# Kernel tuning notes

Hardware: AMD Instinct MI355X
Metric: run time of the kernel (lower is better)

## Reference

```python
import jax, jax.numpy as jnp
import numpy as np

D = 127          # feature dim d
TD = D + 1       # token_dim = d + 1 = 128
H = D            # hidden_dim defaults to d
L = 2            # num_layers
EPS = 1e-6       # block eps
LN_EPS = 1e-5    # torch LayerNorm default


def _layernorm(x, w, b):
    m = jnp.mean(x, axis=-1, keepdims=True)
    v = jnp.mean(jnp.square(x - m), axis=-1, keepdims=True)
    return (x - m) * jax.lax.rsqrt(v + LN_EPS) * w + b


def _phi(x):
    return jax.nn.elu(x) + 1.0


def _gla_block(tokens, wq, wk, wv, wg_w, wg_b, wo, l1w, l1b, l2w, l2b):
    # tokens: (B, T, TD)
    x = _layernorm(tokens, l1w, l1b)
    Q = x @ wq.T                      # (B,T,H)
    K = x @ wk.T                      # (B,T,H)
    V = x @ wv.T                      # (B,T,TD)
    G = jax.nn.sigmoid(x @ wg_w.T + wg_b)
    Vg = V * G
    Qp = _phi(Q)
    Kp = _phi(K)
    # causal linear attention via cumulative outer-product state
    kv = jnp.einsum('bth,btm->bthm', Kp, Vg)   # (B,T,H,TD)
    S_kv = jnp.cumsum(kv, axis=1)
    S_k = jnp.cumsum(Kp, axis=1)
    numerator = jnp.einsum('bth,bthm->btm', Qp, S_kv)   # (B,T,TD)
    denom = jnp.maximum(jnp.einsum('bth,bth->bt', Qp, S_k), EPS)
    attn_out = numerator / denom[..., None]
    out = tokens + (attn_out @ wo.T) * 0.1
    return _layernorm(out, l2w, l2b)


def setup_inputs() -> dict:
    key = jax.random.key(0)
    ks = jax.random.split(key, 16)
    B, N = 2, 4095
    s = 0.02  # small xavier-ish gain used by the module
    inp = {
        'xs': jax.random.normal(ks[0], (B, N, D), jnp.float32),
        'ys': jax.random.normal(ks[1], (B, N), jnp.float32),
        'query_x': jax.random.normal(ks[2], (B, 1, D), jnp.float32),
        'Wq': jax.random.normal(ks[3], (L, H, TD), jnp.float32) * s,
        'Wk': jax.random.normal(ks[4], (L, H, TD), jnp.float32) * s,
        'Wv': jax.random.normal(ks[5], (L, TD, TD), jnp.float32) * s,
        'Wg_w': jax.random.normal(ks[6], (L, TD, TD), jnp.float32) * s,
        'Wg_b': jnp.zeros((L, TD), jnp.float32),
        'Wo': jax.random.normal(ks[7], (L, TD, TD), jnp.float32) * s,
        'ln1_w': jnp.ones((L, TD), jnp.float32),
        'ln1_b': jnp.zeros((L, TD), jnp.float32),
        'ln2_w': jnp.ones((L, TD), jnp.float32),
        'ln2_b': jnp.zeros((L, TD), jnp.float32),
        'pred_w': jax.random.normal(ks[8], (1, TD), jnp.float32) * 0.1,
    }
    return inp


def reference(xs, ys, query_x, Wq, Wk, Wv, Wg_w, Wg_b, Wo,
              ln1_w, ln1_b, ln2_w, ln2_b, pred_w):
    B = xs.shape[0]
    train_tokens = jnp.concatenate([xs, ys[..., None]], axis=-1)       # (B,N,TD)
    query_token = jnp.concatenate(
        [query_x, jnp.zeros((B, 1, 1), xs.dtype)], axis=-1)            # (B,1,TD)
    tokens = jnp.concatenate([train_tokens, query_token], axis=1)      # (B,T,TD)
    for l in range(L):
        tokens = _gla_block(tokens, Wq[l], Wk[l], Wv[l], Wg_w[l], Wg_b[l],
                            Wo[l], ln1_w[l], ln1_b[l], ln2_w[l], ln2_b[l])
    y_pred = tokens[:, -1, :] @ pred_w.T   # (B,1)
    return y_pred[:, 0]
```

## Files before the change

kernel.cpp:

```cpp
#include <hip/hip_runtime.h>
#include <hip/hip_bf16.h>

#define TT 4096
#define NCH 32
#define BB 2

__device__ float g_tok[(size_t)BB*TT*128];
__device__ float g_xn [(size_t)BB*TT*128];
__device__ float g_Qp [(size_t)BB*TT*128];
__device__ float g_Kp [(size_t)BB*TT*128];
__device__ float g_Vg [(size_t)BB*TT*128];
__device__ float g_Pv [(size_t)BB*TT*128];
__device__ float g_Pg [(size_t)BB*TT*128];
__device__ float g_Ssum[(size_t)BB*NCH*16384];
__device__ float g_Spre[(size_t)BB*NCH*16384];
__device__ float g_Sk [(size_t)BB*NCH*128];
__device__ float g_Skp[(size_t)BB*NCH*128];

__device__ __forceinline__ float phi_f(float x){ return x > 0.f ? x + 1.f : __expf(x); }
__device__ __forceinline__ float sigm_f(float x){ return 1.f/(1.f+__expf(-x)); }

__global__ __launch_bounds__(256) void k0_build(const float* __restrict__ xs,
                                                const float* __restrict__ ys,
                                                const float* __restrict__ qx){
  long e = (long)blockIdx.x * 256 + threadIdx.x;
  int col = (int)(e & 127);
  long r = e >> 7;
  int t = (int)(r & (TT-1));
  int b = (int)(r >> 12);
  float v;
  if (t < TT-1) {
    v = (col < 127) ? xs[((long)b*(TT-1) + t)*127 + col] : ys[(long)b*(TT-1) + t];
  } else {
    v = (col < 127) ? qx[(long)b*127 + col] : 0.f;
  }
  g_tok[e] = v;
}

__global__ __launch_bounds__(256) void k1a_ln(const float* __restrict__ lnw,
                                              const float* __restrict__ lnb){
  int tid = threadIdx.x;
  long r0 = (long)blockIdx.x * 8;
  int row = tid >> 5;
  int col = (tid & 31) << 2;
  float4 v = *(const float4*)(g_tok + (r0 + row)*128 + col);
  float s1 = v.x+v.y+v.z+v.w;
  float s2 = v.x*v.x+v.y*v.y+v.z*v.z+v.w*v.w;
  #pragma unroll
  for (int off=1; off<32; off<<=1){ s1 += __shfl_xor(s1,off); s2 += __shfl_xor(s2,off); }
  float mean = s1*(1.f/128.f);
  float var  = s2*(1.f/128.f) - mean*mean;
  float rstd = rsqrtf(var + 1e-5f);
  float4 w4 = *(const float4*)(lnw+col);
  float4 b4 = *(const float4*)(lnb+col);
  float4 o;
  o.x = (v.x-mean)*rstd*w4.x + b4.x;
  o.y = (v.y-mean)*rstd*w4.y + b4.y;
  o.z = (v.z-mean)*rstd*w4.z + b4.z;
  o.w = (v.w-mean)*rstd*w4.w + b4.w;
  *(float4*)(g_xn + (r0 + row)*128 + col) = o;
}

__global__ __launch_bounds__(256) void k1b_gemm(
    const float* __restrict__ Wq, const float* __restrict__ Wk,
    const float* __restrict__ Wv, const float* __restrict__ Wg)
{
  __shared__ float xt[128*132];
  __shared__ float wt[128*132];
  int tid = threadIdx.x;
  int mat = blockIdx.x & 3;
  long row0 = (long)(blockIdx.x >> 2) * 128;
  const float* W = (mat==0) ? Wq : (mat==1) ? Wk : (mat==2) ? Wv : Wg;
  bool isQK = (mat < 2);
  for (int i=0;i<16;i++){
    int ts = (tid & 31) + 32*(i & 3);
    int hc = (tid >> 5) + 8*(i >> 2);
    float4 v = *(const float4*)(g_xn + (row0+ts)*128 + hc*4);
    xt[(hc*4+0)*132+ts] = v.x;
    xt[(hc*4+1)*132+ts] = v.y;
    xt[(hc*4+2)*132+ts] = v.z;
    xt[(hc*4+3)*132+ts] = v.w;
  }
  for (int i=0;i<16;i++){
    int ts = (tid & 31) + 32*(i & 3);
    int hc = (tid >> 5) + 8*(i >> 2);
    int wr = isQK ? (ts < 127 ? ts : 126) : ts;
    float4 v = *(const float4*)(W + (long)wr*128 + hc*4);
    wt[(hc*4+0)*132+ts] = v.x;
    wt[(hc*4+1)*132+ts] = v.y;
    wt[(hc*4+2)*132+ts] = v.z;
    wt[(hc*4+3)*132+ts] = v.w;
  }
  __syncthreads();
  int r0 = (tid >> 4) * 8;
  int c0 = (tid & 15) * 8;
  float acc[8][8];
  #pragma unroll
  for (int i=0;i<8;i++)
    #pragma unroll
    for (int j=0;j<8;j++) acc[i][j]=0.f;
  for (int k=0;k<128;k++){
    float4 xa = *(const float4*)&xt[k*132 + r0];
    float4 xb = *(const float4*)&xt[k*132 + r0 + 4];
    float4 wa = *(const float4*)&wt[k*132 + c0];
    float4 wb = *(const float4*)&wt[k*132 + c0 + 4];
    float xr[8] = {xa.x,xa.y,xa.z,xa.w,xb.x,xb.y,xb.z,xb.w};
    float wc[8] = {wa.x,wa.y,wa.z,wa.w,wb.x,wb.y,wb.z,wb.w};
    #pragma unroll
    for (int i=0;i<8;i++)
      #pragma unroll
      for (int j=0;j<8;j++)
        acc[i][j] += xr[i]*wc[j];
  }
  long rbase = row0 + r0;
  if (isQK){
    float* dst = (mat==0) ? g_Qp : g_Kp;
    #pragma unroll
    for (int i=0;i<8;i++){
      float v[8];
      #pragma unroll
      for (int j=0;j<8;j++) v[j] = (c0+j < 127) ? phi_f(acc[i][j]) : 0.f;
      *(float4*)(dst + (rbase+i)*128 + c0)     = make_float4(v[0],v[1],v[2],v[3]);
      *(float4*)(dst + (rbase+i)*128 + c0 + 4) = make_float4(v[4],v[5],v[6],v[7]);
    }
  } else {
    float* dst = (mat==2) ? g_Pv : g_Pg;
    #pragma unroll
    for (int i=0;i<8;i++){
      *(float4*)(dst + (rbase+i)*128 + c0)     = make_float4(acc[i][0],acc[i][1],acc[i][2],acc[i][3]);
      *(float4*)(dst + (rbase+i)*128 + c0 + 4) = make_float4(acc[i][4],acc[i][5],acc[i][6],acc[i][7]);
    }
  }
}

__global__ __launch_bounds__(256) void k1c_vg(const float* __restrict__ Wgb){
  long e = ((long)blockIdx.x*256 + threadIdx.x) * 4;
  int j = (int)(e & 127);
  float4 pv = *(const float4*)(g_Pv + e);
  float4 pg = *(const float4*)(g_Pg + e);
  float4 gb = *(const float4*)(Wgb + j);
  float4 o;
  o.x = pv.x * sigm_f(pg.x + gb.x);
  o.y = pv.y * sigm_f(pg.y + gb.y);
  o.z = pv.z * sigm_f(pg.z + gb.z);
  o.w = pv.w * sigm_f(pg.w + gb.w);
  *(float4*)(g_Vg + e) = o;
}

__global__ __launch_bounds__(256) void k2_chunksum()
{
  __shared__ float vgs[16][128];
  __shared__ float kps[16][32];
  int tid = threadIdx.x;
  int ht = blockIdx.x & 3;
  int c  = (blockIdx.x >> 2) & 31;
  int b  = blockIdx.x >> 7;
  int hl = tid >> 3, mg = tid & 7, m0 = mg << 4;
  int h  = ht*32 + hl;
  float acc[16];
  #pragma unroll
  for (int i=0;i<16;i++) acc[i]=0.f;
  float sk = 0.f;
  long base = ((long)b*TT + c*128)*128;
  for (int tb=0; tb<8; tb++){
    __syncthreads();
    { int e = tid*8; int ts = e >> 7; int cc = e & 127;
      const float* s = g_Vg + base + (long)(tb*16+ts)*128 + cc;
      *(float4*)&vgs[ts][cc]   = *(const float4*)s;
      *(float4*)&vgs[ts][cc+4] = *(const float4*)(s+4); }
    { int e = tid*2; int ts = e >> 5; int hh = e & 31;
      const float* s = g_Kp + base + (long)(tb*16+ts)*128 + ht*32 + hh;
      kps[ts][hh] = s[0]; kps[ts][hh+1] = s[1]; }
    __syncthreads();
    for (int ts=0; ts<16; ts++){
      float kp = kps[ts][hl];
      sk += kp;
      #pragma unroll
      for (int i=0;i<16;i++) acc[i] += kp * vgs[ts][m0+i];
    }
  }
  long so = (((long)b*NCH + c)*128 + h)*128 + m0;
  #pragma unroll
  for (int i=0;i<16;i+=4)
    *(float4*)(g_Ssum + so + i) = make_float4(acc[i],acc[i+1],acc[i+2],acc[i+3]);
  if (mg==0) g_Sk[((long)b*NCH + c)*128 + h] = sk;
}

__global__ __launch_bounds__(256) void k3_scan()
{
  int blk = blockIdx.x % 65;
  int b   = blockIdx.x / 65;
  if (blk < 64){
    int e = blk*256 + threadIdx.x;
    float a = 0.f;
    for (int c=0;c<NCH;c++){
      long idx = ((long)b*NCH + c)*16384 + e;
      g_Spre[idx] = a;
      a += g_Ssum[idx];
    }
  } else if (threadIdx.x < 128){
    int e = threadIdx.x;
    float a = 0.f;
    for (int c=0;c<NCH;c++){
      long idx = ((long)b*NCH + c)*128 + e;
      g_Skp[idx] = a;
      a += g_Sk[idx];
    }
  }
}

__global__ __launch_bounds__(256) void k4_fused(
    const float* __restrict__ Wo,
    const float* __restrict__ ln2w, const float* __restrict__ ln2b)
{
  __shared__ float spl[16384];
  __shared__ float ktl[128*132];
  __shared__ float bufb[32*132];
  __shared__ float skl[128];
  int tid = threadIdx.x;
  int rq = blockIdx.x & 3;
  int c  = (blockIdx.x >> 2) & 31;
  int b  = blockIdx.x >> 7;
  int r0 = rq*32;
  long cbase = ((long)b*TT + c*128)*128;
  long sbase = ((long)b*NCH + c)*16384;

  for (int i=0;i<16;i++){
    int e = i*1024 + tid*4;
    *(float4*)&spl[e] = *(const float4*)(g_Spre + sbase + e);
  }
  if (tid < 128) skl[tid] = g_Skp[((long)b*NCH + c)*128 + tid];
  for (int i=0;i<4;i++){
    int e = i*1024 + tid*4;
    int row = e >> 7, cc = e & 127;
    *(float4*)&bufb[row*132+cc] = *(const float4*)(g_Qp + cbase + (long)(r0+row)*128 + cc);
  }
  for (int i=0;i<16;i++){
    int ts = (tid & 31) + 32*(i & 3);
    int hc = (tid >> 5) + 8*(i >> 2);
    float4 v = *(const float4*)(g_Kp + cbase + (long)ts*128 + hc*4);
    ktl[(hc*4+0)*132 + ts] = v.x;
    ktl[(hc*4+1)*132 + ts] = v.y;
    ktl[(hc*4+2)*132 + ts] = v.z;
    ktl[(hc*4+3)*132 + ts] = v.w;
  }
  __syncthreads();

  int row_l = tid >> 3, cg = tid & 7;
  int tq = r0 + row_l;
  long trow = (long)b*TT + c*128 + tq;
  float acc2[16], a[16];
  #pragma unroll
  for (int i=0;i<16;i++){ acc2[i]=0.f; a[i]=0.f; }
  float den_i = 0.f;
  for (int h=0;h<128;h++){
    float qv = bufb[row_l*132 + h];
    den_i += qv * skl[h];
    #pragma unroll
    for (int j=0;j<4;j++){
      float4 s4 = *(const float4*)&spl[h*128 + cg*4 + 32*j];
      float4 k4 = *(const float4*)&ktl[h*132 + cg*4 + 32*j];
      acc2[4*j+0] += qv*s4.x; acc2[4*j+1] += qv*s4.y; acc2[4*j+2] += qv*s4.z; acc2[4*j+3] += qv*s4.w;
      a[4*j+0]    += qv*k4.x; a[4*j+1]    += qv*k4.y; a[4*j+2]    += qv*k4.z; a[4*j+3]    += qv*k4.w;
    }
  }
  float den_a = 0.f;
  #pragma unroll
  for (int j=0;j<4;j++){
    #pragma unroll
    for (int k=0;k<4;k++){
      int ts = cg*4 + 32*j + k;
      if (ts > tq) a[4*j+k] = 0.f;
      den_a += a[4*j+k];
    }
  }
  den_a += __shfl_xor(den_a, 1);
  den_a += __shfl_xor(den_a, 2);
  den_a += __shfl_xor(den_a, 4);
  float inv = 1.f / fmaxf(den_i + den_a, 1e-6f);
  __syncthreads();
  #pragma unroll
  for (int j=0;j<4;j++)
    *(float4*)&bufb[row_l*132 + cg*4 + 32*j] = make_float4(a[4*j],a[4*j+1],a[4*j+2],a[4*j+3]);
  for (int i=0;i<16;i++){
    int e = i*1024 + tid*4;
    *(float4*)&ktl[e] = *(const float4*)(g_Vg + cbase + e);
  }
  __syncthreads();
  for (int ts=0; ts<128; ts++){
    float av = bufb[row_l*132 + ts];
    #pragma unroll
    for (int j=0;j<4;j++){
      float4 v4 = *(const float4*)&ktl[ts*128 + cg*4 + 32*j];
      acc2[4*j+0]+=av*v4.x; acc2[4*j+1]+=av*v4.y; acc2[4*j+2]+=av*v4.z; acc2[4*j+3]+=av*v4.w;
    }
  }
  __syncthreads();
  #pragma unroll
  for (int j=0;j<4;j++)
    *(float4*)&bufb[row_l*132 + cg*4 + 32*j] =
      make_float4(acc2[4*j]*inv, acc2[4*j+1]*inv, acc2[4*j+2]*inv, acc2[4*j+3]*inv);
  for (int i=0;i<16;i++){
    int n  = (tid & 31) + 32*(i & 3);
    int mc = (tid >> 5) + 8*(i >> 2);
    float4 v = *(const float4*)(Wo + (long)n*128 + mc*4);
    ktl[(mc*4+0)*132 + n] = v.x;
    ktl[(mc*4+1)*132 + n] = v.y;
    ktl[(mc*4+2)*132 + n] = v.z;
    ktl[(mc*4+3)*132 + n] = v.w;
  }
  __syncthreads();
  float s[16];
  #pragma unroll
  for (int i=0;i<16;i++) s[i]=0.f;
  for (int m=0;m<128;m++){
    float av = bufb[row_l*132 + m];
    #pragma unroll
    for (int j=0;j<4;j++){
      float4 w4 = *(const float4*)&ktl[m*132 + cg*4 + 32*j];
      s[4*j+0]+=av*w4.x; s[4*j+1]+=av*w4.y; s[4*j+2]+=av*w4.z; s[4*j+3]+=av*w4.w;
    }
  }
  float outv[16];
  float s1=0.f, s2=0.f;
  #pragma unroll
  for (int j=0;j<4;j++){
    float4 t4 = *(const float4*)(g_tok + trow*128 + cg*4 + 32*j);
    outv[4*j+0] = t4.x + 0.1f*s[4*j+0];
    outv[4*j+1] = t4.y + 0.1f*s[4*j+1];
    outv[4*j+2] = t4.z + 0.1f*s[4*j+2];
    outv[4*j+3] = t4.w + 0.1f*s[4*j+3];
  }
  #pragma unroll
  for (int i=0;i<16;i++){ s1 += outv[i]; s2 += outv[i]*outv[i]; }
  s1 += __shfl_xor(s1,1); s2 += __shfl_xor(s2,1);
  s1 += __shfl_xor(s1,2); s2 += __shfl_xor(s2,2);
  s1 += __shfl_xor(s1,4); s2 += __shfl_xor(s2,4);
  float mean = s1*(1.f/128.f);
  float var  = s2*(1.f/128.f) - mean*mean;
  float rstd = rsqrtf(var + 1e-5f);
  #pragma unroll
  for (int j=0;j<4;j++){
    int n = cg*4 + 32*j;
    float4 w4 = *(const float4*)(ln2w+n);
    float4 b4 = *(const float4*)(ln2b+n);
    float4 o;
    o.x = (outv[4*j+0]-mean)*rstd*w4.x + b4.x;
    o.y = (outv[4*j+1]-mean)*rstd*w4.y + b4.y;
    o.z = (outv[4*j+2]-mean)*rstd*w4.z + b4.z;
    o.w = (outv[4*j+3]-mean)*rstd*w4.w + b4.w;
    *(float4*)(g_tok + trow*128 + n) = o;
  }
}

__global__ __launch_bounds__(128) void k5_pred(const float* __restrict__ pw,
                                               float* __restrict__ out){
  __shared__ float red[2];
  int b = blockIdx.x, tid = threadIdx.x;
  float v = g_tok[((long)b*TT + TT-1)*128 + tid] * pw[tid];
  #pragma unroll
  for (int off=1; off<64; off<<=1) v += __shfl_xor(v, off);
  if ((tid & 63) == 0) red[tid>>6] = v;
  __syncthreads();
  if (tid==0) out[b] = red[0] + red[1];
}

extern "C" void kernel_launch(void* const* d_in, const int* in_sizes, int n_in,
                              void* d_out, int out_size, void* d_ws, size_t ws_size,
                              hipStream_t stream)
{
  (void)in_sizes; (void)n_in; (void)out_size; (void)d_ws; (void)ws_size;
  const float* xs   = (const float*)d_in[0];
  const float* ys   = (const float*)d_in[1];
  const float* qx   = (const float*)d_in[2];
  const float* Wq   = (const float*)d_in[3];
  const float* Wk   = (const float*)d_in[4];
  const float* Wv   = (const float*)d_in[5];
  const float* Wgw  = (const float*)d_in[6];
  const float* Wgb  = (const float*)d_in[7];
  const float* Wo   = (const float*)d_in[8];
  const float* ln1w = (const float*)d_in[9];
  const float* ln1b = (const float*)d_in[10];
  const float* ln2w = (const float*)d_in[11];
  const float* ln2b = (const float*)d_in[12];
  const float* predw= (const float*)d_in[13];

  k0_build<<<4096, 256, 0, stream>>>(xs, ys, qx);

  for (int l=0; l<2; l++){
    const float* Wq_l  = Wq  + (size_t)l*127*128;
    const float* Wk_l  = Wk  + (size_t)l*127*128;
    const float* Wv_l  = Wv  + (size_t)l*128*128;
    const float* Wgw_l = Wgw + (size_t)l*128*128;
    const float* Wgb_l = Wgb + (size_t)l*128;
    const float* Wo_l  = Wo  + (size_t)l*128*128;
    const float* l1w = ln1w + (size_t)l*128;
    const float* l1b = ln1b + (size_t)l*128;
    const float* l2w = ln2w + (size_t)l*128;
    const float* l2b = ln2b + (size_t)l*128;

    k1a_ln<<<1024, 256, 0, stream>>>(l1w, l1b);
    k1b_gemm<<<256, 256, 0, stream>>>(Wq_l, Wk_l, Wv_l, Wgw_l);
    k1c_vg<<<1024, 256, 0, stream>>>(Wgb_l);
    k2_chunksum<<<256, 256, 0, stream>>>();
    k3_scan<<<130, 256, 0, stream>>>();
    k4_fused<<<256, 256, 0, stream>>>(Wo_l, l2w, l2b);
  }
  k5_pred<<<BB, 128, 0, stream>>>(predw, (float*)d_out);
}
```

Measured before the change: 252.3 us.

## Fuse LayerNorm into projection GEMM and retile fused attention kernel

Removes the standalone LayerNorm kernel by having the projection GEMM load raw tokens, normalize them in shared memory, and use a row-major tile with strided row reads. Each GEMM block now recomputes the LayerNorm for its 128 rows, once per projection matrix. The fused attention kernel is retiled so each thread handles two rows and eight columns split into two halves. Its prefix-state tile is also padded to a 132 stride. This cuts a launch and a global round trip per layer and changes the LDS access pattern, at the cost of fourfold redundant LayerNorm work.

New measurement: 244.3 us. 3.2% less time.

```diff
diff --git a/kernel.cpp b/kernel.cpp
--- a/kernel.cpp
+++ b/kernel.cpp
@@ -6,7 +6,6 @@
 #define BB 2
 
 __device__ float g_tok[(size_t)BB*TT*128];
-__device__ float g_xn [(size_t)BB*TT*128];
 __device__ float g_Qp [(size_t)BB*TT*128];
 __device__ float g_Kp [(size_t)BB*TT*128];
 __device__ float g_Vg [(size_t)BB*TT*128];
@@ -37,35 +36,12 @@
   g_tok[e] = v;
 }
 
-__global__ __launch_bounds__(256) void k1a_ln(const float* __restrict__ lnw,
-                                              const float* __restrict__ lnb){
-  int tid = threadIdx.x;
-  long r0 = (long)blockIdx.x * 8;
-  int row = tid >> 5;
-  int col = (tid & 31) << 2;
-  float4 v = *(const float4*)(g_tok + (r0 + row)*128 + col);
-  float s1 = v.x+v.y+v.z+v.w;
-  float s2 = v.x*v.x+v.y*v.y+v.z*v.z+v.w*v.w;
-  #pragma unroll
-  for (int off=1; off<32; off<<=1){ s1 += __shfl_xor(s1,off); s2 += __shfl_xor(s2,off); }
-  float mean = s1*(1.f/128.f);
-  float var  = s2*(1.f/128.f) - mean*mean;
-  float rstd = rsqrtf(var + 1e-5f);
-  float4 w4 = *(const float4*)(lnw+col);
-  float4 b4 = *(const float4*)(lnb+col);
-  float4 o;
-  o.x = (v.x-mean)*rstd*w4.x + b4.x;
-  o.y = (v.y-mean)*rstd*w4.y + b4.y;
-  o.z = (v.z-mean)*rstd*w4.z + b4.z;
-  o.w = (v.w-mean)*rstd*w4.w + b4.w;
-  *(float4*)(g_xn + (r0 + row)*128 + col) = o;
-}
-
 __global__ __launch_bounds__(256) void k1b_gemm(
     const float* __restrict__ Wq, const float* __restrict__ Wk,
-    const float* __restrict__ Wv, const float* __restrict__ Wg)
+    const float* __restrict__ Wv, const float* __restrict__ Wg,
+    const float* __restrict__ lnw, const float* __restrict__ lnb)
 {
-  __shared__ float xt[128*132];
+  __shared__ float xl[128*132];
   __shared__ float wt[128*132];
   int tid = threadIdx.x;
   int mat = blockIdx.x & 3;
@@ -75,15 +51,6 @@
   for (int i=0;i<16;i++){
     int ts = (tid & 31) + 32*(i & 3);
     int hc = (tid >> 5) + 8*(i >> 2);
-    float4 v = *(const float4*)(g_xn + (row0+ts)*128 + hc*4);
-    xt[(hc*4+0)*132+ts] = v.x;
-    xt[(hc*4+1)*132+ts] = v.y;
-    xt[(hc*4+2)*132+ts] = v.z;
-    xt[(hc*4+3)*132+ts] = v.w;
-  }
-  for (int i=0;i<16;i++){
-    int ts = (tid & 31) + 32*(i & 3);
-    int hc = (tid >> 5) + 8*(i >> 2);
     int wr = isQK ? (ts < 127 ? ts : 126) : ts;
     float4 v = *(const float4*)(W + (long)wr*128 + hc*4);
     wt[(hc*4+0)*132+ts] = v.x;
@@ -91,20 +58,45 @@
     wt[(hc*4+2)*132+ts] = v.z;
     wt[(hc*4+3)*132+ts] = v.w;
   }
-  __syncthreads();
-  int r0 = (tid >> 4) * 8;
-  int c0 = (tid & 15) * 8;
+  {
+    int row = tid >> 1, half = tid & 1;
+    const float* src = g_tok + (row0 + row)*128 + half*64;
+    float s1 = 0.f, s2 = 0.f;
+    for (int u=0; u<16; u++){
+      float4 v = *(const float4*)(src + u*4);
+      s1 += v.x+v.y+v.z+v.w;
+      s2 += v.x*v.x+v.y*v.y+v.z*v.z+v.w*v.w;
+      *(float4*)&xl[row*132 + half*64 + u*4] = v;
+    }
+    s1 += __shfl_xor(s1, 1); s2 += __shfl_xor(s2, 1);
+    float mean = s1*(1.f/128.f);
+    float var  = s2*(1.f/128.f) - mean*mean;
+    float rstd = rsqrtf(var + 1e-5f);
+    for (int u=0; u<16; u++){
+      int cc = half*64 + u*4;
+      float4 v  = *(float4*)&xl[row*132 + cc];
+      float4 w4 = *(const float4*)(lnw + cc);
+      float4 b4 = *(const float4*)(lnb + cc);
+      v.x = (v.x-mean)*rstd*w4.x + b4.x;
+      v.y = (v.y-mean)*rstd*w4.y + b4.y;
+      v.z = (v.z-mean)*rstd*w4.z + b4.z;
+      v.w = (v.w-mean)*rstd*w4.w + b4.w;
+      *(float4*)&xl[row*132 + cc] = v;
+    }
+  }
+  __syncthreads();
+  int g = tid >> 4, c = tid & 15;
   float acc[8][8];
   #pragma unroll
   for (int i=0;i<8;i++)
     #pragma unroll
     for (int j=0;j<8;j++) acc[i][j]=0.f;
   for (int k=0;k<128;k++){
-    float4 xa = *(const float4*)&xt[k*132 + r0];
-    float4 xb = *(const float4*)&xt[k*132 + r0 + 4];
-    float4 wa = *(const float4*)&wt[k*132 + c0];
-    float4 wb = *(const float4*)&wt[k*132 + c0 + 4];
-    float xr[8] = {xa.x,xa.y,xa.z,xa.w,xb.x,xb.y,xb.z,xb.w};
+    float xr[8];
+    #pragma unroll
+    for (int i=0;i<8;i++) xr[i] = xl[(g+16*i)*132 + k];
+    float4 wa = *(const float4*)&wt[k*132 + c*4];
+    float4 wb = *(const float4*)&wt[k*132 + 64 + c*4];
     float wc[8] = {wa.x,wa.y,wa.z,wa.w,wb.x,wb.y,wb.z,wb.w};
     #pragma unroll
     for (int i=0;i<8;i++)
@@ -112,23 +104,29 @@
       for (int j=0;j<8;j++)
         acc[i][j] += xr[i]*wc[j];
   }
-  long rbase = row0 + r0;
   if (isQK){
     float* dst = (mat==0) ? g_Qp : g_Kp;
     #pragma unroll
     for (int i=0;i<8;i++){
-      float v[8];
+      long rr = row0 + g + 16*i;
+      float v0[4], v1[4];
       #pragma unroll
-      for (int j=0;j<8;j++) v[j] = (c0+j < 127) ? phi_f(acc[i][j]) : 0.f;
-      *(float4*)(dst + (rbase+i)*128 + c0)     = make_float4(v[0],v[1],v[2],v[3]);
-      *(float4*)(dst + (rbase+i)*128 + c0 + 4) = make_float4(v[4],v[5],v[6],v[7]);
+      for (int j=0;j<4;j++) v0[j] = phi_f(acc[i][j]);
+      #pragma unroll
+      for (int j=0;j<4;j++){
+        int col = 64 + c*4 + j;
+        v1[j] = (col < 127) ? phi_f(acc[i][4+j]) : 0.f;
+      }
+      *(float4*)(dst + rr*128 + c*4)      = make_float4(v0[0],v0[1],v0[2],v0[3]);
+      *(float4*)(dst + rr*128 + 64 + c*4) = make_float4(v1[0],v1[1],v1[2],v1[3]);
     }
   } else {
     float* dst = (mat==2) ? g_Pv : g_Pg;
     #pragma unroll
     for (int i=0;i<8;i++){
-      *(float4*)(dst + (rbase+i)*128 + c0)     = make_float4(acc[i][0],acc[i][1],acc[i][2],acc[i][3]);
-      *(float4*)(dst + (rbase+i)*128 + c0 + 4) = make_float4(acc[i][4],acc[i][5],acc[i][6],acc[i][7]);
+      long rr = row0 + g + 16*i;
+      *(float4*)(dst + rr*128 + c*4)      = make_float4(acc[i][0],acc[i][1],acc[i][2],acc[i][3]);
+      *(float4*)(dst + rr*128 + 64 + c*4) = make_float4(acc[i][4],acc[i][5],acc[i][6],acc[i][7]);
     }
   }
 }
@@ -213,7 +211,7 @@
     const float* __restrict__ Wo,
     const float* __restrict__ ln2w, const float* __restrict__ ln2b)
 {
-  __shared__ float spl[16384];
+  __shared__ float spl[128*132];
   __shared__ float ktl[128*132];
   __shared__ float bufb[32*132];
   __shared__ float skl[128];
@@ -227,7 +225,8 @@
 
   for (int i=0;i<16;i++){
     int e = i*1024 + tid*4;
-    *(float4*)&spl[e] = *(const float4*)(g_Spre + sbase + e);
+    int h = e >> 7, n = e & 127;
+    *(float4*)&spl[h*132+n] = *(const float4*)(g_Spre + sbase + e);
   }
   if (tid < 128) skl[tid] = g_Skp[((long)b*NCH + c)*128 + tid];
   for (int i=0;i<4;i++){
@@ -246,60 +245,72 @@
   }
   __syncthreads();
 
-  int row_l = tid >> 3, cg = tid & 7;
-  int tq = r0 + row_l;
-  long trow = (long)b*TT + c*128 + tq;
-  float acc2[16], a[16];
-  #pragma unroll
-  for (int i=0;i<16;i++){ acc2[i]=0.f; a[i]=0.f; }
-  float den_i = 0.f;
+  int rp = tid >> 4, cg = tid & 15;
+  int rl0 = rp*2, rl1 = rp*2+1;
+  int tq0 = r0 + rl0, tq1 = r0 + rl1;
+  float acc2[2][8], a[2][8];
+  #pragma unroll
+  for (int r=0;r<2;r++)
+    #pragma unroll
+    for (int j=0;j<8;j++){ acc2[r][j]=0.f; a[r][j]=0.f; }
+  float den0 = 0.f, den1 = 0.f;
   for (int h=0;h<128;h++){
-    float qv = bufb[row_l*132 + h];
-    den_i += qv * skl[h];
-    #pragma unroll
-    for (int j=0;j<4;j++){
-      float4 s4 = *(const float4*)&spl[h*128 + cg*4 + 32*j];
-      float4 k4 = *(const float4*)&ktl[h*132 + cg*4 + 32*j];
-      acc2[4*j+0] += qv*s4.x; acc2[4*j+1] += qv*s4.y; acc2[4*j+2] += qv*s4.z; acc2[4*j+3] += qv*s4.w;
-      a[4*j+0]    += qv*k4.x; a[4*j+1]    += qv*k4.y; a[4*j+2]    += qv*k4.z; a[4*j+3]    += qv*k4.w;
-    }
-  }
-  float den_a = 0.f;
-  #pragma unroll
-  for (int j=0;j<4;j++){
-    #pragma unroll
-    for (int k=0;k<4;k++){
-      int ts = cg*4 + 32*j + k;
-      if (ts > tq) a[4*j+k] = 0.f;
-      den_a += a[4*j+k];
-    }
-  }
-  den_a += __shfl_xor(den_a, 1);
-  den_a += __shfl_xor(den_a, 2);
-  den_a += __shfl_xor(den_a, 4);
-  float inv = 1.f / fmaxf(den_i + den_a, 1e-6f);
-  __syncthreads();
-  #pragma unroll
-  for (int j=0;j<4;j++)
-    *(float4*)&bufb[row_l*132 + cg*4 + 32*j] = make_float4(a[4*j],a[4*j+1],a[4*j+2],a[4*j+3]);
+    float q0 = bufb[rl0*132 + h];
+    float q1 = bufb[rl1*132 + h];
+    float sv = skl[h];
+    den0 += q0*sv; den1 += q1*sv;
+    float4 sa = *(const float4*)&spl[h*132 + cg*4];
+    float4 sb = *(const float4*)&spl[h*132 + 64 + cg*4];
+    float4 ka = *(const float4*)&ktl[h*132 + cg*4];
+    float4 kb = *(const float4*)&ktl[h*132 + 64 + cg*4];
+    acc2[0][0]+=q0*sa.x; acc2[0][1]+=q0*sa.y; acc2[0][2]+=q0*sa.z; acc2[0][3]+=q0*sa.w;
+    acc2[0][4]+=q0*sb.x; acc2[0][5]+=q0*sb.y; acc2[0][6]+=q0*sb.z; acc2[0][7]+=q0*sb.w;
+    acc2[1][0]+=q1*sa.x; acc2[1][1]+=q1*sa.y; acc2[1][2]+=q1*sa.z; acc2[1][3]+=q1*sa.w;
+    acc2[1][4]+=q1*sb.x; acc2[1][5]+=q1*sb.y; acc2[1][6]+=q1*sb.z; acc2[1][7]+=q1*sb.w;
+    a[0][0]+=q0*ka.x; a[0][1]+=q0*ka.y; a[0][2]+=q0*ka.z; a[0][3]+=q0*ka.w;
+    a[0][4]+=q0*kb.x; a[0][5]+=q0*kb.y; a[0][6]+=q0*kb.z; a[0][7]+=q0*kb.w;
+    a[1][0]+=q1*ka.x; a[1][1]+=q1*ka.y; a[1][2]+=q1*ka.z; a[1][3]+=q1*ka.w;
+    a[1][4]+=q1*kb.x; a[1][5]+=q1*kb.y; a[1][6]+=q1*kb.z; a[1][7]+=q1*kb.w;
+  }
+  float dena0 = 0.f, dena1 = 0.f;
+  #pragma unroll
+  for (int j=0;j<8;j++){
+    int ts = (j<4) ? (cg*4+j) : (64 + cg*4 + j-4);
+    if (ts > tq0) a[0][j] = 0.f;
+    if (ts > tq1) a[1][j] = 0.f;
+    dena0 += a[0][j]; dena1 += a[1][j];
+  }
+  dena0 += __shfl_xor(dena0,1); dena1 += __shfl_xor(dena1,1);
+  dena0 += __shfl_xor(dena0,2); dena1 += __shfl_xor(dena1,2);
+  dena0 += __shfl_xor(dena0,4); dena1 += __shfl_xor(dena1,4);
+  dena0 += __shfl_xor(dena0,8); dena1 += __shfl_xor(dena1,8);
+  float inv0 = 1.f / fmaxf(den0 + dena0, 1e-6f);
+  float inv1 = 1.f / fmaxf(den1 + dena1, 1e-6f);
+  __syncthreads();
+  *(float4*)&bufb[rl0*132 + cg*4]      = make_float4(a[0][0],a[0][1],a[0][2],a[0][3]);
+  *(float4*)&bufb[rl0*132 + 64 + cg*4] = make_float4(a[0][4],a[0][5],a[0][6],a[0][7]);
+  *(float4*)&bufb[rl1*132 + cg*4]      = make_float4(a[1][0],a[1][1],a[1][2],a[1][3]);
+  *(float4*)&bufb[rl1*132 + 64 + cg*4] = make_float4(a[1][4],a[1][5],a[1][6],a[1][7]);
   for (int i=0;i<16;i++){
     int e = i*1024 + tid*4;
     *(float4*)&ktl[e] = *(const float4*)(g_Vg + cbase + e);
   }
   __syncthreads();
   for (int ts=0; ts<128; ts++){
-    float av = bufb[row_l*132 + ts];
-    #pragma unroll
-    for (int j=0;j<4;j++){
-      float4 v4 = *(const float4*)&ktl[ts*128 + cg*4 + 32*j];
-      acc2[4*j+0]+=av*v4.x; acc2[4*j+1]+=av*v4.y; acc2[4*j+2]+=av*v4.z; acc2[4*j+3]+=av*v4.w;
-    }
-  }
-  __syncthreads();
-  #pragma unroll
-  for (int j=0;j<4;j++)
-    *(float4*)&bufb[row_l*132 + cg*4 + 32*j] =
-      make_float4(acc2[4*j]*inv, acc2[4*j+1]*inv, acc2[4*j+2]*inv, acc2[4*j+3]*inv);
+    float a0 = bufb[rl0*132 + ts];
+    float a1 = bufb[rl1*132 + ts];
+    float4 va = *(const float4*)&ktl[ts*128 + cg*4];
+    float4 vb = *(const float4*)&ktl[ts*128 + 64 + cg*4];
+    acc2[0][0]+=a0*va.x; acc2[0][1]+=a0*va.y; acc2[0][2]+=a0*va.z; acc2[0][3]+=a0*va.w;
+    acc2[0][4]+=a0*vb.x; acc2[0][5]+=a0*vb.y; acc2[0][6]+=a0*vb.z; acc2[0][7]+=a0*vb.w;
+    acc2[1][0]+=a1*va.x; acc2[1][1]+=a1*va.y; acc2[1][2]+=a1*va.z; acc2[1][3]+=a1*va.w;
+    acc2[1][4]+=a1*vb.x; acc2[1][5]+=a1*vb.y; acc2[1][6]+=a1*vb.z; acc2[1][7]+=a1*vb.w;
+  }
+  __syncthreads();
+  *(float4*)&bufb[rl0*132 + cg*4]      = make_float4(acc2[0][0]*inv0,acc2[0][1]*inv0,acc2[0][2]*inv0,acc2[0][3]*inv0);
+  *(float4*)&bufb[rl0*132 + 64 + cg*4] = make_float4(acc2[0][4]*inv0,acc2[0][5]*inv0,acc2[0][6]*inv0,acc2[0][7]*inv0);
+  *(float4*)&bufb[rl1*132 + cg*4]      = make_float4(acc2[1][0]*inv1,acc2[1][1]*inv1,acc2[1][2]*inv1,acc2[1][3]*inv1);
+  *(float4*)&bufb[rl1*132 + 64 + cg*4] = make_float4(acc2[1][4]*inv1,acc2[1][5]*inv1,acc2[1][6]*inv1,acc2[1][7]*inv1);
   for (int i=0;i<16;i++){
     int n  = (tid & 31) + 32*(i & 3);
     int mc = (tid >> 5) + 8*(i >> 2);
@@ -310,46 +321,66 @@
     ktl[(mc*4+3)*132 + n] = v.w;
   }
   __syncthreads();
-  float s[16];
-  #pragma unroll
-  for (int i=0;i<16;i++) s[i]=0.f;
+  float s[2][8];
+  #pragma unroll
+  for (int r=0;r<2;r++)
+    #pragma unroll
+    for (int j=0;j<8;j++) s[r][j]=0.f;
   for (int m=0;m<128;m++){
-    float av = bufb[row_l*132 + m];
-    #pragma unroll
-    for (int j=0;j<4;j++){
-      float4 w4 = *(const float4*)&ktl[m*132 + cg*4 + 32*j];
-      s[4*j+0]+=av*w4.x; s[4*j+1]+=av*w4.y; s[4*j+2]+=av*w4.z; s[4*j+3]+=av*w4.w;
-    }
-  }
-  float outv[16];
-  float s1=0.f, s2=0.f;
-  #pragma unroll
-  for (int j=0;j<4;j++){
-    float4 t4 = *(const float4*)(g_tok + trow*128 + cg*4 + 32*j);
-    outv[4*j+0] = t4.x + 0.1f*s[4*j+0];
-    outv[4*j+1] = t4.y + 0.1f*s[4*j+1];
-    outv[4*j+2] = t4.z + 0.1f*s[4*j+2];
-    outv[4*j+3] = t4.w + 0.1f*s[4*j+3];
-  }
-  #pragma unroll
-  for (int i=0;i<16;i++){ s1 += outv[i]; s2 += outv[i]*outv[i]; }
-  s1 += __shfl_xor(s1,1); s2 += __shfl_xor(s2,1);
-  s1 += __shfl_xor(s1,2); s2 += __shfl_xor(s2,2);
-  s1 += __shfl_xor(s1,4); s2 += __shfl_xor(s2,4);
-  float mean = s1*(1.f/128.f);
-  float var  = s2*(1.f/128.f) - mean*mean;
-  float rstd = rsqrtf(var + 1e-5f);
-  #pragma unroll
-  for (int j=0;j<4;j++){
-    int n = cg*4 + 32*j;
+    float a0 = bufb[rl0*132 + m];
+    float a1 = bufb[rl1*132 + m];
+    float4 wa = *(const float4*)&ktl[m*132 + cg*4];
+    float4 wb = *(const float4*)&ktl[m*132 + 64 + cg*4];
+    s[0][0]+=a0*wa.x; s[0][1]+=a0*wa.y; s[0][2]+=a0*wa.z; s[0][3]+=a0*wa.w;
+    s[0][4]+=a0*wb.x; s[0][5]+=a0*wb.y; s[0][6]+=a0*wb.z; s[0][7]+=a0*wb.w;
+    s[1][0]+=a1*wa.x; s[1][1]+=a1*wa.y; s[1][2]+=a1*wa.z; s[1][3]+=a1*wa.w;
+    s[1][4]+=a1*wb.x; s[1][5]+=a1*wb.y; s[1][6]+=a1*wb.z; s[1][7]+=a1*wb.w;
+  }
+  long trow0 = (long)b*TT + c*128 + tq0;
+  long trow1 = (long)b*TT + c*128 + tq1;
+  float outv[2][8];
+  {
+    float4 t0a = *(const float4*)(g_tok + trow0*128 + cg*4);
+    float4 t0b = *(const float4*)(g_tok + trow0*128 + 64 + cg*4);
+    float4 t1a = *(const float4*)(g_tok + trow1*128 + cg*4);
+    float4 t1b = *(const float4*)(g_tok + trow1*128 + 64 + cg*4);
+    outv[0][0]=t0a.x+0.1f*s[0][0]; outv[0][1]=t0a.y+0.1f*s[0][1];
+    outv[0][2]=t0a.z+0.1f*s[0][2]; outv[0][3]=t0a.w+0.1f*s[0][3];
+    outv[0][4]=t0b.x+0.1f*s[0][4]; outv[0][5]=t0b.y+0.1f*s[0][5];
+    outv[0][6]=t0b.z+0.1f*s[0][6]; outv[0][7]=t0b.w+0.1f*s[0][7];
+    outv[1][0]=t1a.x+0.1f*s[1][0]; outv[1][1]=t1a.y+0.1f*s[1][1];
+    outv[1][2]=t1a.z+0.1f*s[1][2]; outv[1][3]=t1a.w+0.1f*s[1][3];
+    outv[1][4]=t1b.x+0.1f*s[1][4]; outv[1][5]=t1b.y+0.1f*s[1][5];
+    outv[1][6]=t1b.z+0.1f*s[1][6]; outv[1][7]=t1b.w+0.1f*s[1][7];
+  }
+  float s10=0.f, s20=0.f, s11=0.f, s21=0.f;
+  #pragma unroll
+  for (int j=0;j<8;j++){
+    s10 += outv[0][j]; s20 += outv[0][j]*outv[0][j];
+    s11 += outv[1][j]; s21 += outv[1][j]*outv[1][j];
+  }
+  s10 += __shfl_xor(s10,1); s20 += __shfl_xor(s20,1); s11 += __shfl_xor(s11,1); s21 += __shfl_xor(s21,1);
+  s10 += __shfl_xor(s10,2); s20 += __shfl_xor(s20,2); s11 += __shfl_xor(s11,2); s21 += __shfl_xor(s21,2);
+  s10 += __shfl_xor(s10,4); s20 += __shfl_xor(s20,4); s11 += __shfl_xor(s11,4); s21 += __shfl_xor(s21,4);
+  s10 += __shfl_xor(s10,8); s20 += __shfl_xor(s20,8); s11 += __shfl_xor(s11,8); s21 += __shfl_xor(s21,8);
+  float mean0 = s10*(1.f/128.f), var0 = s20*(1.f/128.f)-mean0*mean0, rstd0 = rsqrtf(var0+1e-5f);
+  float mean1 = s11*(1.f/128.f), var1 = s21*(1.f/128.f)-mean1*mean1, rstd1 = rsqrtf(var1+1e-5f);
+  #pragma unroll
+  for (int half=0; half<2; half++){
+    int n = half*64 + cg*4;
     float4 w4 = *(const float4*)(ln2w+n);
     float4 b4 = *(const float4*)(ln2b+n);
-    float4 o;
-    o.x = (outv[4*j+0]-mean)*rstd*w4.x + b4.x;
-    o.y = (outv[4*j+1]-mean)*rstd*w4.y + b4.y;
-    o.z = (outv[4*j+2]-mean)*rstd*w4.z + b4.z;
-    o.w = (outv[4*j+3]-mean)*rstd*w4.w + b4.w;
-    *(float4*)(g_tok + trow*128 + n) = o;
+    float4 o0, o1;
+    o0.x=(outv[0][half*4+0]-mean0)*rstd0*w4.x+b4.x;
+    o0.y=(outv[0][half*4+1]-mean0)*rstd0*w4.y+b4.y;
+    o0.z=(outv[0][half*4+2]-mean0)*rstd0*w4.z+b4.z;
+    o0.w=(outv[0][half*4+3]-mean0)*rstd0*w4.w+b4.w;
+    o1.x=(outv[1][half*4+0]-mean1)*rstd1*w4.x+b4.x;
+    o1.y=(outv[1][half*4+1]-mean1)*rstd1*w4.y+b4.y;
+    o1.z=(outv[1][half*4+2]-mean1)*rstd1*w4.z+b4.z;
+    o1.w=(outv[1][half*4+3]-mean1)*rstd1*w4.w+b4.w;
+    *(float4*)(g_tok + trow0*128 + n) = o0;
+    *(float4*)(g_tok + trow1*128 + n) = o1;
   }
 }
 
@@ -399,8 +430,7 @@
     const float* l2w = ln2w + (size_t)l*128;
     const float* l2b = ln2b + (size_t)l*128;
 
-    k1a_ln<<<1024, 256, 0, stream>>>(l1w, l1b);
-    k1b_gemm<<<256, 256, 0, stream>>>(Wq_l, Wk_l, Wv_l, Wgw_l);
+    k1b_gemm<<<256, 256, 0, stream>>>(Wq_l, Wk_l, Wv_l, Wgw_l, l1w, l1b);
     k1c_vg<<<1024, 256, 0, stream>>>(Wgb_l);
     k2_chunksum<<<256, 256, 0, stream>>>();
     k3_scan<<<130, 256, 0, stream>>>();
```
